# Performance work log

Measured on AMD Instinct MI355X. Metric: run time of the kernel, lower is better.

Reference implementation:

```python
import jax, jax.numpy as jnp
import numpy as np
import math

EMBED_DIM = 1024
NUM_HEADS = 16
HEAD_DIM = EMBED_DIM // NUM_HEADS


def setup_inputs() -> dict:
    key = jax.random.key(0)
    ks = jax.random.split(key, 5)
    s = 1.0 / math.sqrt(EMBED_DIM)
    return {
        "x": jax.random.normal(ks[0], (2, 2048, EMBED_DIM), dtype=jnp.float32),
        "w_qkv": jax.random.normal(ks[1], (EMBED_DIM, 3 * EMBED_DIM), dtype=jnp.float32) * s,
        "b_qkv": jax.random.normal(ks[2], (3 * EMBED_DIM,), dtype=jnp.float32) * 0.01,
        "w_proj": jax.random.normal(ks[3], (EMBED_DIM, EMBED_DIM), dtype=jnp.float32) * s,
        "b_proj": jax.random.normal(ks[4], (EMBED_DIM,), dtype=jnp.float32) * 0.01,
    }


def reference(x, w_qkv, b_qkv, w_proj, b_proj):
    B, T, C = x.shape
    qkv = (x @ w_qkv + b_qkv).reshape(B, T, 3, NUM_HEADS, HEAD_DIM)
    q, k, v = qkv[:, :, 0], qkv[:, :, 1], qkv[:, :, 2]  # [B,T,H,D]
    # scores: [B,H,T,T]
    att = jnp.einsum("bqhd,bkhd->bhqk", q, k) / math.sqrt(HEAD_DIM)
    causal = jnp.tril(jnp.ones((T, T), dtype=bool))
    att = jnp.where(causal[None, None], att, -jnp.inf)
    att = jax.nn.softmax(att, axis=-1)
    out = jnp.einsum("bhqk,bkhd->bqhd", att, v).reshape(B, T, C)
    return out @ w_proj + b_proj
```

## Files before the change

### kernel.cpp

```cpp
#include <hip/hip_runtime.h>
#include <stdint.h>


#define B_  2
#define T_  2048
#define C_  1024
#define NH  16
#define HD  64
#define BH_ (B_*NH)
#define M_  (B_*T_)

typedef __attribute__((ext_vector_type(8))) short short8;
typedef __attribute__((ext_vector_type(4))) float f32x4;
typedef __attribute__((ext_vector_type(4))) uint32_t u32x4;

struct frag2 { short8 hi, lo; };

typedef const __attribute__((address_space(1))) void* gas_ptr;
typedef __attribute__((address_space(3))) void* las_ptr;

__device__ __forceinline__ void gload_lds16(const void* g, void* l) {
  __builtin_amdgcn_global_load_lds((gas_ptr)g, (las_ptr)l, 16, 0, 0);
}

__device__ __forceinline__ uint32_t packsplit(float x) {
  uint32_t u = __float_as_uint(x);
  uint32_t hib = u & 0xffff0000u;
  float r = x - __uint_as_float(hib);
  uint32_t v = __float_as_uint(r);
  uint32_t lo = (v + 0x7fffu + ((v >> 16) & 1u)) >> 16;
  return hib | lo;
}

__device__ __forceinline__ frag2 extract2(u32x4 a, u32x4 b) {
  union U { u32x4 u; short8 s; };
  U H, L;
  H.u[0] = __builtin_amdgcn_perm(a[1], a[0], 0x07060302u);
  H.u[1] = __builtin_amdgcn_perm(a[3], a[2], 0x07060302u);
  H.u[2] = __builtin_amdgcn_perm(b[1], b[0], 0x07060302u);
  H.u[3] = __builtin_amdgcn_perm(b[3], b[2], 0x07060302u);
  L.u[0] = __builtin_amdgcn_perm(a[1], a[0], 0x05040100u);
  L.u[1] = __builtin_amdgcn_perm(a[3], a[2], 0x05040100u);
  L.u[2] = __builtin_amdgcn_perm(b[1], b[0], 0x05040100u);
  L.u[3] = __builtin_amdgcn_perm(b[3], b[2], 0x05040100u);
  frag2 f; f.hi = H.s; f.lo = L.s; return f;
}

__device__ __forceinline__ f32x4 mfma16(short8 a, short8 b, f32x4 c) {
  return __builtin_amdgcn_mfma_f32_16x16x32_bf16(a, b, c, 0, 0, 0);
}


__global__ __launch_bounds__(256) void pack4_kernel(const float4* __restrict__ in,
                                                    u32x4* __restrict__ out, int n4) {
  int i = blockIdx.x * 256 + threadIdx.x;
  if (i < n4) {
    float4 v = in[i];
    u32x4 p;
    p[0] = packsplit(v.x); p[1] = packsplit(v.y);
    p[2] = packsplit(v.z); p[3] = packsplit(v.w);
    out[i] = p;
  }
}

__global__ __launch_bounds__(1024) void pack_t_kernel(const float* __restrict__ in,
                                                      uint32_t* __restrict__ out, int R, int C) {
  __shared__ float tile[64][65];
  int c0 = blockIdx.x * 64, r0 = blockIdx.y * 64;
  int tx = threadIdx.x, ty = threadIdx.y;
  #pragma unroll
  for (int i = 0; i < 4; ++i)
    tile[ty + 16*i][tx] = in[(size_t)(r0 + ty + 16*i)*C + c0 + tx];
  __syncthreads();
  #pragma unroll
  for (int i = 0; i < 4; ++i)
    out[(size_t)(c0 + ty + 16*i)*R + r0 + tx] = packsplit(tile[tx][ty + 16*i]);
}


template<int MODE>
__global__ __launch_bounds__(256) void gemm_split(const uint32_t* __restrict__ A,
                                                  const uint32_t* __restrict__ Bt,
                                                  const float* __restrict__ bias,
                                                  uint32_t* __restrict__ qp,
                                                  uint32_t* __restrict__ kp,
                                                  uint32_t* __restrict__ vtp,
                                                  float* __restrict__ fout,
                                                  int M, int N, int K) {
  __shared__ uint32_t As[128*8*4];
  __shared__ uint32_t Bs[128*8*4];
  int tid = threadIdx.x;
  int w = tid >> 6, l = tid & 63, lg = l >> 4, lr = l & 15;
  int bm = blockIdx.y * 128, bn = blockIdx.x * 128;
  int wm = (w >> 1) * 64, wn = (w & 1) * 64;
  f32x4 zero = {0.f, 0.f, 0.f, 0.f};
  f32x4 acc[4][4];
  #pragma unroll
  for (int i = 0; i < 4; ++i)
    #pragma unroll
    for (int j = 0; j < 4; ++j) acc[i][j] = zero;

  for (int k0 = 0; k0 < K; k0 += 32) {
    #pragma unroll
    for (int i = 0; i < 4; ++i) {
      int s = tid + 256*i;
      int row = s >> 3, k4 = s & 7;
      int g4 = k4 ^ (row & 7);
      gload_lds16(A  + (size_t)(bm + row)*K + k0 + g4*4, &As[s*4]);
      gload_lds16(Bt + (size_t)(bn + row)*K + k0 + g4*4, &Bs[s*4]);
    }
    __syncthreads();
    frag2 af[4];
    #pragma unroll
    for (int mf = 0; mf < 4; ++mf) {
      int row = wm + mf*16 + lr;
      int sb = row*8;
      int s0 = sb + ((2*lg)   ^ (row & 7));
      int s1 = sb + ((2*lg+1) ^ (row & 7));
      af[mf] = extract2(*(const u32x4*)&As[s0*4], *(const u32x4*)&As[s1*4]);
    }
    #pragma unroll
    for (int nf = 0; nf < 4; ++nf) {
      int row = wn + nf*16 + lr;
      int sb = row*8;
      int s0 = sb + ((2*lg)   ^ (row & 7));
      int s1 = sb + ((2*lg+1) ^ (row & 7));
      frag2 bfr = extract2(*(const u32x4*)&Bs[s0*4], *(const u32x4*)&Bs[s1*4]);
      #pragma unroll
      for (int mf = 0; mf < 4; ++mf) {
        acc[mf][nf] = mfma16(af[mf].hi, bfr.hi, acc[mf][nf]);
        acc[mf][nf] = mfma16(af[mf].hi, bfr.lo, acc[mf][nf]);
        acc[mf][nf] = mfma16(af[mf].lo, bfr.hi, acc[mf][nf]);
      }
    }
    __syncthreads();
  }
  #pragma unroll
  for (int nf = 0; nf < 4; ++nf) {
    int col = bn + wn + nf*16 + lr;
    float bv = bias[col];
    #pragma unroll
    for (int mf = 0; mf < 4; ++mf) {
      #pragma unroll
      for (int r = 0; r < 4; ++r) {
        int rowm = bm + wm + mf*16 + lg*4 + r;
        float v = acc[mf][nf][r] + bv;
        if (MODE == 1) {
          fout[(size_t)rowm*N + col] = v;
        } else {
          int sec = col >> 10;
          int hh  = (col >> 6) & 15;
          int d   = col & 63;
          int b   = rowm >> 11, t = rowm & 2047;
          uint32_t pkv = packsplit(v);
          size_t bhh = (size_t)b*NH + hh;
          if (sec == 0)      qp[(bhh*T_ + t)*HD + d]  = pkv;
          else if (sec == 1) kp[(bhh*T_ + t)*HD + d]  = pkv;
          else               vtp[(bhh*HD + d)*T_ + t] = pkv;
        }
      }
    }
  }
}


__global__ __launch_bounds__(256) void attn_kernel(const uint32_t* __restrict__ qp,
                                                   const uint32_t* __restrict__ kp,
                                                   const uint32_t* __restrict__ vtp,
                                                   uint32_t* __restrict__ ctx) {
  __shared__ uint32_t Kt[64*16*4];
  __shared__ uint32_t Vt[64*16*4];
  __shared__ uint32_t Pl[4][16*68];
  int qt = blockIdx.x, bh = blockIdx.y;
  int tid = threadIdx.x;
  int w = tid >> 6, l = tid & 63, lg = l >> 4, lr = l & 15;
  int q0 = qt * 64;
  const uint32_t* qb = qp + ((size_t)bh*T_ + q0 + w*16 + lr)*HD;
  frag2 qf[2];
  #pragma unroll
  for (int ks = 0; ks < 2; ++ks) {
    u32x4 a = *(const u32x4*)(qb + ks*32 + lg*8);
    u32x4 b = *(const u32x4*)(qb + ks*32 + lg*8 + 4);
    qf[ks] = extract2(a, b);
  }
  f32x4 zero = {0.f, 0.f, 0.f, 0.f};
  f32x4 o[4] = {zero, zero, zero, zero};
  float m_r[4] = {-1e30f, -1e30f, -1e30f, -1e30f};
  float l_r[4] = {0.f, 0.f, 0.f, 0.f};
  uint32_t* pw = &Pl[w][0];

  for (int kt = 0; kt <= qt; ++kt) {
    int kv0 = kt * 64;
    #pragma unroll
    for (int i = 0; i < 4; ++i) {
      int s = tid + 256*i;
      int row = s >> 4, k4 = s & 15;
      int g4 = k4 ^ (row & 7);
      gload_lds16(kp  + ((size_t)bh*T_ + kv0 + row)*HD + g4*4, &Kt[s*4]);
      gload_lds16(vtp + ((size_t)bh*HD + row)*T_ + kv0 + g4*4, &Vt[s*4]);
    }
    __syncthreads();
    f32x4 s4[4];
    #pragma unroll
    for (int fc = 0; fc < 4; ++fc) {
      f32x4 acc = zero;
      #pragma unroll
      for (int ks = 0; ks < 2; ++ks) {
        int row = fc*16 + lr;
        int sb = row*16 + ks*8;
        int s0 = sb + ((2*lg)   ^ (row & 7));
        int s1 = sb + ((2*lg+1) ^ (row & 7));
        frag2 kf = extract2(*(const u32x4*)&Kt[s0*4], *(const u32x4*)&Kt[s1*4]);
        acc = mfma16(qf[ks].hi, kf.hi, acc);
        acc = mfma16(qf[ks].hi, kf.lo, acc);
        acc = mfma16(qf[ks].lo, kf.hi, acc);
      }
      s4[fc] = acc * 0.125f;
    }
    if (kt == qt) {
      #pragma unroll
      for (int fc = 0; fc < 4; ++fc)
        #pragma unroll
        for (int r = 0; r < 4; ++r) {
          int col = kv0 + fc*16 + lr;
          int rw  = q0 + w*16 + lg*4 + r;
          if (col > rw) s4[fc][r] = -1e30f;
        }
    }
    float sc[4];
    #pragma unroll
    for (int r = 0; r < 4; ++r) {
      float v = fmaxf(fmaxf(s4[0][r], s4[1][r]), fmaxf(s4[2][r], s4[3][r]));
      v = fmaxf(v, __shfl_xor(v, 1));
      v = fmaxf(v, __shfl_xor(v, 2));
      v = fmaxf(v, __shfl_xor(v, 4));
      v = fmaxf(v, __shfl_xor(v, 8));
      float mn = fmaxf(m_r[r], v);
      sc[r] = __expf(m_r[r] - mn);
      m_r[r] = mn;
    }
    float sum[4] = {0.f, 0.f, 0.f, 0.f};
    #pragma unroll
    for (int fc = 0; fc < 4; ++fc)
      #pragma unroll
      for (int r = 0; r < 4; ++r) {
        float p = __expf(s4[fc][r] - m_r[r]);
        s4[fc][r] = p;
        sum[r] += p;
      }
    #pragma unroll
    for (int r = 0; r < 4; ++r) {
      float v = sum[r];
      v += __shfl_xor(v, 1); v += __shfl_xor(v, 2);
      v += __shfl_xor(v, 4); v += __shfl_xor(v, 8);
      l_r[r] = l_r[r]*sc[r] + v;
    }
    #pragma unroll
    for (int df = 0; df < 4; ++df)
      #pragma unroll
      for (int r = 0; r < 4; ++r) o[df][r] *= sc[r];
    #pragma unroll
    for (int fc = 0; fc < 4; ++fc)
      #pragma unroll
      for (int r = 0; r < 4; ++r)
        pw[(lg*4 + r)*68 + fc*16 + lr] = packsplit(s4[fc][r]);
    __builtin_amdgcn_sched_barrier(0);
    frag2 pf[2];
    #pragma unroll
    for (int ks = 0; ks < 2; ++ks) {
      const uint32_t* pr = pw + lr*68 + ks*32 + lg*8;
      pf[ks] = extract2(*(const u32x4*)pr, *(const u32x4*)(pr + 4));
    }
    #pragma unroll
    for (int df = 0; df < 4; ++df) {
      #pragma unroll
      for (int ks = 0; ks < 2; ++ks) {
        int row = df*16 + lr;
        int sb = row*16 + ks*8;
        int s0 = sb + ((2*lg)   ^ (row & 7));
        int s1 = sb + ((2*lg+1) ^ (row & 7));
        frag2 vf = extract2(*(const u32x4*)&Vt[s0*4], *(const u32x4*)&Vt[s1*4]);
        o[df] = mfma16(pf[ks].hi, vf.hi, o[df]);
        o[df] = mfma16(pf[ks].hi, vf.lo, o[df]);
        o[df] = mfma16(pf[ks].lo, vf.hi, o[df]);
      }
    }
    __syncthreads();
  }
  int b = bh >> 4, h = bh & 15;
  float inv[4];
  #pragma unroll
  for (int r = 0; r < 4; ++r) inv[r] = 1.0f / l_r[r];
  #pragma unroll
  for (int df = 0; df < 4; ++df)
    #pragma unroll
    for (int r = 0; r < 4; ++r) {
      int q = q0 + w*16 + lg*4 + r;
      ctx[((size_t)b*T_ + q)*C_ + h*HD + df*16 + lr] = packsplit(o[df][r] * inv[r]);
    }
}


extern "C" void kernel_launch(void* const* d_in, const int* in_sizes, int n_in,
                              void* d_out, int out_size, void* d_ws, size_t ws_size,
                              hipStream_t stream) {
  (void)in_sizes; (void)n_in; (void)out_size; (void)ws_size;
  const float* x      = (const float*)d_in[0];
  const float* w_qkv  = (const float*)d_in[1];
  const float* b_qkv  = (const float*)d_in[2];
  const float* w_proj = (const float*)d_in[3];
  const float* b_proj = (const float*)d_in[4];
  float* out = (float*)d_out;

  uint8_t* ws = (uint8_t*)d_ws;
  const size_t MB = (size_t)1 << 20;
  uint32_t* xp  = (uint32_t*)(ws + 0);
  uint32_t* ctx = xp;
  uint32_t* wqt = (uint32_t*)(ws + 16*MB);
  uint32_t* wpt = (uint32_t*)(ws + 28*MB);
  uint32_t* qp  = (uint32_t*)(ws + 32*MB);
  uint32_t* kp  = (uint32_t*)(ws + 48*MB);
  uint32_t* vtp = (uint32_t*)(ws + 64*MB);

  pack4_kernel<<<(M_*C_/4 + 255)/256, 256, 0, stream>>>((const float4*)x, (u32x4*)xp, M_*C_/4);
  pack_t_kernel<<<dim3(3*C_/64, C_/64), dim3(64, 16), 0, stream>>>(w_qkv, wqt, C_, 3*C_);
  pack_t_kernel<<<dim3(C_/64, C_/64), dim3(64, 16), 0, stream>>>(w_proj, wpt, C_, C_);
  gemm_split<0><<<dim3(3*C_/128, M_/128), 256, 0, stream>>>(
      xp, wqt, b_qkv, qp, kp, vtp, nullptr, M_, 3*C_, C_);
  attn_kernel<<<dim3(T_/64, BH_), 256, 0, stream>>>(qp, kp, vtp, ctx);
  gemm_split<1><<<dim3(C_/128, M_/128), 256, 0, stream>>>(
      ctx, wpt, b_proj, nullptr, nullptr, nullptr, out, M_, C_, C_);
}
```

Before: 412.9 us.

## Store split-bf16 operands as separate hi/lo planes and double-buffer attention KV

Operands were packed as interleaved hi/lo bf16 pairs in 32-bit words and unpacked with perm instructions. They are now kept in separate hi and lo bf16 planes, so MFMA fragments load straight from LDS without extraction. The attention kernel also double-buffers K/V tiles in LDS, folds the 1/sqrt(d) scale into Q at the QKV epilogue, and remaps blocks so causal-heavy query tiles launch first with heads grouped per XCD. P is kept as fp32 in LDS and split using the hardware bf16 convert, at the cost of more LDS use and more separate 16-bit global stores.

```diff
diff --git a/kernel.cpp b/kernel.cpp
--- a/kernel.cpp
+++ b/kernel.cpp
@@ -14,8 +14,6 @@
 typedef __attribute__((ext_vector_type(4))) float f32x4;
 typedef __attribute__((ext_vector_type(4))) uint32_t u32x4;
 
-struct frag2 { short8 hi, lo; };
-
 typedef const __attribute__((address_space(1))) void* gas_ptr;
 typedef __attribute__((address_space(3))) void* las_ptr;
 
@@ -23,27 +21,40 @@
   __builtin_amdgcn_global_load_lds((gas_ptr)g, (las_ptr)l, 16, 0, 0);
 }
 
-__device__ __forceinline__ uint32_t packsplit(float x) {
-  uint32_t u = __float_as_uint(x);
-  uint32_t hib = u & 0xffff0000u;
-  float r = x - __uint_as_float(hib);
-  uint32_t v = __float_as_uint(r);
-  uint32_t lo = (v + 0x7fffu + ((v >> 16) & 1u)) >> 16;
-  return hib | lo;
-}
-
-__device__ __forceinline__ frag2 extract2(u32x4 a, u32x4 b) {
-  union U { u32x4 u; short8 s; };
-  U H, L;
+__device__ __forceinline__ unsigned short rne16(float x){
+  uint32_t v = __float_as_uint(x);
+  return (unsigned short)((v + 0x7fffu + ((v >> 16) & 1u)) >> 16);
+}
+
+__device__ __forceinline__ uint32_t cvtpk_bf16(float a, float b){
+  uint32_t r;
+  asm("v_cvt_pk_bf16_f32 %0, %1, %2" : "=v"(r) : "v"(a), "v"(b));
+  return r;
+}
+
+__device__ __forceinline__ short8 hi8(u32x4 a, u32x4 b){
+  union { u32x4 u; short8 s; } H;
   H.u[0] = __builtin_amdgcn_perm(a[1], a[0], 0x07060302u);
   H.u[1] = __builtin_amdgcn_perm(a[3], a[2], 0x07060302u);
   H.u[2] = __builtin_amdgcn_perm(b[1], b[0], 0x07060302u);
   H.u[3] = __builtin_amdgcn_perm(b[3], b[2], 0x07060302u);
-  L.u[0] = __builtin_amdgcn_perm(a[1], a[0], 0x05040100u);
-  L.u[1] = __builtin_amdgcn_perm(a[3], a[2], 0x05040100u);
-  L.u[2] = __builtin_amdgcn_perm(b[1], b[0], 0x05040100u);
-  L.u[3] = __builtin_amdgcn_perm(b[3], b[2], 0x05040100u);
-  frag2 f; f.hi = H.s; f.lo = L.s; return f;
+  return H.s;
+}
+__device__ __forceinline__ short8 lo8(u32x4 a, u32x4 b){
+  float l0 = __uint_as_float(a[0]) - __uint_as_float(a[0] & 0xffff0000u);
+  float l1 = __uint_as_float(a[1]) - __uint_as_float(a[1] & 0xffff0000u);
+  float l2 = __uint_as_float(a[2]) - __uint_as_float(a[2] & 0xffff0000u);
+  float l3 = __uint_as_float(a[3]) - __uint_as_float(a[3] & 0xffff0000u);
+  float l4 = __uint_as_float(b[0]) - __uint_as_float(b[0] & 0xffff0000u);
+  float l5 = __uint_as_float(b[1]) - __uint_as_float(b[1] & 0xffff0000u);
+  float l6 = __uint_as_float(b[2]) - __uint_as_float(b[2] & 0xffff0000u);
+  float l7 = __uint_as_float(b[3]) - __uint_as_float(b[3] & 0xffff0000u);
+  union { u32x4 u; short8 s; } L;
+  L.u[0] = cvtpk_bf16(l0, l1);
+  L.u[1] = cvtpk_bf16(l2, l3);
+  L.u[2] = cvtpk_bf16(l4, l5);
+  L.u[3] = cvtpk_bf16(l6, l7);
+  return L.s;
 }
 
 __device__ __forceinline__ f32x4 mfma16(short8 a, short8 b, f32x4 c) {
@@ -52,19 +63,31 @@
 
 
 __global__ __launch_bounds__(256) void pack4_kernel(const float4* __restrict__ in,
-                                                    u32x4* __restrict__ out, int n4) {
+                                                    unsigned short* __restrict__ oh,
+                                                    unsigned short* __restrict__ ol, int n4) {
   int i = blockIdx.x * 256 + threadIdx.x;
   if (i < n4) {
     float4 v = in[i];
-    u32x4 p;
-    p[0] = packsplit(v.x); p[1] = packsplit(v.y);
-    p[2] = packsplit(v.z); p[3] = packsplit(v.w);
-    out[i] = p;
+    float f[4] = {v.x, v.y, v.z, v.w};
+    ushort4 h, lo;
+    unsigned short hh[4], ll[4];
+    #pragma unroll
+    for (int j=0;j<4;++j){
+      uint32_t bt = __float_as_uint(f[j]);
+      hh[j] = (unsigned short)(bt >> 16);
+      ll[j] = rne16(f[j] - __uint_as_float(bt & 0xffff0000u));
+    }
+    h.x=hh[0]; h.y=hh[1]; h.z=hh[2]; h.w=hh[3];
+    lo.x=ll[0]; lo.y=ll[1]; lo.z=ll[2]; lo.w=ll[3];
+    *(ushort4*)(oh + (size_t)i*4) = h;
+    *(ushort4*)(ol + (size_t)i*4) = lo;
   }
 }
 
 __global__ __launch_bounds__(1024) void pack_t_kernel(const float* __restrict__ in,
-                                                      uint32_t* __restrict__ out, int R, int C) {
+                                                      unsigned short* __restrict__ oh,
+                                                      unsigned short* __restrict__ ol,
+                                                      int R, int C) {
   __shared__ float tile[64][65];
   int c0 = blockIdx.x * 64, r0 = blockIdx.y * 64;
   int tx = threadIdx.x, ty = threadIdx.y;
@@ -73,26 +96,46 @@
     tile[ty + 16*i][tx] = in[(size_t)(r0 + ty + 16*i)*C + c0 + tx];
   __syncthreads();
   #pragma unroll
-  for (int i = 0; i < 4; ++i)
-    out[(size_t)(c0 + ty + 16*i)*R + r0 + tx] = packsplit(tile[tx][ty + 16*i]);
+  for (int i = 0; i < 4; ++i) {
+    float v = tile[tx][ty + 16*i];
+    uint32_t bt = __float_as_uint(v);
+    size_t o = (size_t)(c0 + ty + 16*i)*R + r0 + tx;
+    oh[o] = (unsigned short)(bt >> 16);
+    ol[o] = rne16(v - __uint_as_float(bt & 0xffff0000u));
+  }
 }
 
 
 template<int MODE>
-__global__ __launch_bounds__(256) void gemm_split(const uint32_t* __restrict__ A,
-                                                  const uint32_t* __restrict__ Bt,
-                                                  const float* __restrict__ bias,
-                                                  uint32_t* __restrict__ qp,
-                                                  uint32_t* __restrict__ kp,
-                                                  uint32_t* __restrict__ vtp,
-                                                  float* __restrict__ fout,
-                                                  int M, int N, int K) {
-  __shared__ uint32_t As[128*8*4];
-  __shared__ uint32_t Bs[128*8*4];
+__global__ __launch_bounds__(256) void gemm_planes(
+    const unsigned short* __restrict__ Ah, const unsigned short* __restrict__ Al,
+    const unsigned short* __restrict__ Bh, const unsigned short* __restrict__ Bl,
+    const float* __restrict__ bias,
+    unsigned short* __restrict__ qh, unsigned short* __restrict__ ql,
+    unsigned short* __restrict__ kh, unsigned short* __restrict__ kl,
+    unsigned short* __restrict__ vth, unsigned short* __restrict__ vtl,
+    float* __restrict__ fout, int M, int N, int K) {
+  __shared__ unsigned short As[128*64];
+  __shared__ unsigned short Bs[128*64];
   int tid = threadIdx.x;
-  int w = tid >> 6, l = tid & 63, lg = l >> 4, lr = l & 15;
+  int w = tid >> 6, l = tid & 63, lg = l >> 4, lr = l & 15, lr7 = lr & 7;
   int bm = blockIdx.y * 128, bn = blockIdx.x * 128;
   int wm = (w >> 1) * 64, wn = (w & 1) * 64;
+
+  const unsigned short* asrc[4]; const unsigned short* bsrc[4];
+  #pragma unroll
+  for (int i = 0; i < 4; ++i) {
+    int s = tid + 256*i; int r = s >> 3, p = s & 7, u = p ^ (r & 7);
+    asrc[i] = ((u < 4) ? Ah : Al) + (size_t)(bm + r)*K + (u & 3)*8;
+    bsrc[i] = ((u < 4) ? Bh : Bl) + (size_t)(bn + r)*K + (u & 3)*8;
+  }
+  int aoh[4], boh[4];
+  #pragma unroll
+  for (int f = 0; f < 4; ++f) {
+    aoh[f] = (wm + f*16 + lr)*128 + ((lg ^ lr7)*16);
+    boh[f] = (wn + f*16 + lr)*128 + ((lg ^ lr7)*16);
+  }
+
   f32x4 zero = {0.f, 0.f, 0.f, 0.f};
   f32x4 acc[4][4];
   #pragma unroll
@@ -104,33 +147,26 @@
     #pragma unroll
     for (int i = 0; i < 4; ++i) {
       int s = tid + 256*i;
-      int row = s >> 3, k4 = s & 7;
-      int g4 = k4 ^ (row & 7);
-      gload_lds16(A  + (size_t)(bm + row)*K + k0 + g4*4, &As[s*4]);
-      gload_lds16(Bt + (size_t)(bn + row)*K + k0 + g4*4, &Bs[s*4]);
+      gload_lds16(asrc[i], (char*)As + (size_t)s*16);
+      gload_lds16(bsrc[i], (char*)Bs + (size_t)s*16);
+      asrc[i] += 32; bsrc[i] += 32;
     }
     __syncthreads();
-    frag2 af[4];
+    short8 ahf[4], alf[4];
     #pragma unroll
     for (int mf = 0; mf < 4; ++mf) {
-      int row = wm + mf*16 + lr;
-      int sb = row*8;
-      int s0 = sb + ((2*lg)   ^ (row & 7));
-      int s1 = sb + ((2*lg+1) ^ (row & 7));
-      af[mf] = extract2(*(const u32x4*)&As[s0*4], *(const u32x4*)&As[s1*4]);
+      ahf[mf] = *(const short8*)((const char*)As + aoh[mf]);
+      alf[mf] = *(const short8*)((const char*)As + (aoh[mf] ^ 64));
     }
     #pragma unroll
     for (int nf = 0; nf < 4; ++nf) {
-      int row = wn + nf*16 + lr;
-      int sb = row*8;
-      int s0 = sb + ((2*lg)   ^ (row & 7));
-      int s1 = sb + ((2*lg+1) ^ (row & 7));
-      frag2 bfr = extract2(*(const u32x4*)&Bs[s0*4], *(const u32x4*)&Bs[s1*4]);
+      short8 bhf = *(const short8*)((const char*)Bs + boh[nf]);
+      short8 blf = *(const short8*)((const char*)Bs + (boh[nf] ^ 64));
       #pragma unroll
       for (int mf = 0; mf < 4; ++mf) {
-        acc[mf][nf] = mfma16(af[mf].hi, bfr.hi, acc[mf][nf]);
-        acc[mf][nf] = mfma16(af[mf].hi, bfr.lo, acc[mf][nf]);
-        acc[mf][nf] = mfma16(af[mf].lo, bfr.hi, acc[mf][nf]);
+        acc[mf][nf] = mfma16(ahf[mf], bhf, acc[mf][nf]);
+        acc[mf][nf] = mfma16(ahf[mf], blf, acc[mf][nf]);
+        acc[mf][nf] = mfma16(alf[mf], bhf, acc[mf][nf]);
       }
     }
     __syncthreads();
@@ -152,11 +188,14 @@
           int hh  = (col >> 6) & 15;
           int d   = col & 63;
           int b   = rowm >> 11, t = rowm & 2047;
-          uint32_t pkv = packsplit(v);
           size_t bhh = (size_t)b*NH + hh;
-          if (sec == 0)      qp[(bhh*T_ + t)*HD + d]  = pkv;
-          else if (sec == 1) kp[(bhh*T_ + t)*HD + d]  = pkv;
-          else               vtp[(bhh*HD + d)*T_ + t] = pkv;
+          if (sec == 0) v *= 0.125f;
+          uint32_t bt = __float_as_uint(v);
+          unsigned short h16 = (unsigned short)(bt >> 16);
+          unsigned short l16 = rne16(v - __uint_as_float(bt & 0xffff0000u));
+          if (sec == 0)      { size_t o = (bhh*T_ + t)*HD + d;  qh[o] = h16;  ql[o] = l16; }
+          else if (sec == 1) { size_t o = (bhh*T_ + t)*HD + d;  kh[o] = h16;  kl[o] = l16; }
+          else               { size_t o = (bhh*HD + d)*T_ + t;  vth[o] = h16; vtl[o] = l16; }
         }
       }
     }
@@ -164,65 +203,106 @@
 }
 
 
-__global__ __launch_bounds__(256) void attn_kernel(const uint32_t* __restrict__ qp,
-                                                   const uint32_t* __restrict__ kp,
-                                                   const uint32_t* __restrict__ vtp,
-                                                   uint32_t* __restrict__ ctx) {
-  __shared__ uint32_t Kt[64*16*4];
-  __shared__ uint32_t Vt[64*16*4];
-  __shared__ uint32_t Pl[4][16*68];
-  int qt = blockIdx.x, bh = blockIdx.y;
+__global__ __launch_bounds__(256) void attn_kernel(
+    const unsigned short* __restrict__ qh, const unsigned short* __restrict__ ql,
+    const unsigned short* __restrict__ kh, const unsigned short* __restrict__ kl,
+    const unsigned short* __restrict__ vth, const unsigned short* __restrict__ vtl,
+    unsigned short* __restrict__ ctxh, unsigned short* __restrict__ ctxl) {
+  __shared__ unsigned short Kt[2][64*128];
+  __shared__ unsigned short Vt[2][64*128];
+  __shared__ float Pf[4][1024];
+  int bx = blockIdx.x;
+  int xcd = bx & 7, jj = bx >> 3;
+  int bh = xcd*4 + (jj >> 5);
+  int qt = 31 - (jj & 31);
   int tid = threadIdx.x;
-  int w = tid >> 6, l = tid & 63, lg = l >> 4, lr = l & 15;
+  int w = tid >> 6, l = tid & 63, lg = l >> 4, lr = l & 15, lr7 = lr & 7;
   int q0 = qt * 64;
-  const uint32_t* qb = qp + ((size_t)bh*T_ + q0 + w*16 + lr)*HD;
-  frag2 qf[2];
+
+  const unsigned short* qbh = qh + ((size_t)bh*T_ + q0 + w*16 + lr)*HD;
+  const unsigned short* qbl = ql + ((size_t)bh*T_ + q0 + w*16 + lr)*HD;
+  short8 qfh[2], qfl[2];
   #pragma unroll
   for (int ks = 0; ks < 2; ++ks) {
-    u32x4 a = *(const u32x4*)(qb + ks*32 + lg*8);
-    u32x4 b = *(const u32x4*)(qb + ks*32 + lg*8 + 4);
-    qf[ks] = extract2(a, b);
-  }
+    qfh[ks] = *(const short8*)(qbh + ks*32 + lg*8);
+    qfl[ks] = *(const short8*)(qbl + ks*32 + lg*8);
+  }
+
+  const unsigned short* ksrc[4]; const unsigned short* vsrc[4];
+  #pragma unroll
+  for (int i = 0; i < 4; ++i) {
+    int s = tid + 256*i; int r = s >> 4, p = s & 15;
+    int u = (p & 8) | ((p & 7) ^ (r & 7));
+    ksrc[i] = ((u < 8) ? kh : kl) + ((size_t)bh*T_ + r)*HD + (u & 7)*8;
+    vsrc[i] = ((u < 8) ? vth : vtl) + ((size_t)bh*HD + r)*T_ + (u & 7)*8;
+  }
+  auto stage = [&](int buf) {
+    #pragma unroll
+    for (int i = 0; i < 4; ++i) {
+      int s = tid + 256*i;
+      gload_lds16(ksrc[i], (char*)&Kt[buf][0] + (size_t)s*16);
+      gload_lds16(vsrc[i], (char*)&Vt[buf][0] + (size_t)s*16);
+    }
+    #pragma unroll
+    for (int i = 0; i < 4; ++i) { ksrc[i] += 64*HD; vsrc[i] += 64; }
+  };
+
+  int koff[4][2];
+  #pragma unroll
+  for (int fc = 0; fc < 4; ++fc)
+    #pragma unroll
+    for (int ks = 0; ks < 2; ++ks)
+      koff[fc][ks] = (fc*16 + lr)*256 + (((ks*4 + lg) ^ lr7)*16);
+  int pwoff[16];
+  #pragma unroll
+  for (int fc = 0; fc < 4; ++fc)
+    #pragma unroll
+    for (int r = 0; r < 4; ++r) {
+      int q = lg*4 + r;
+      int u = fc*4 + (lr >> 2);
+      pwoff[fc*4 + r] = q*256 + ((u ^ q)*16) + (lr & 3)*4;
+    }
+  int proff[2][2];
+  #pragma unroll
+  for (int ks = 0; ks < 2; ++ks)
+    #pragma unroll
+    for (int g = 0; g < 2; ++g)
+      proff[ks][g] = lr*256 + (((ks*8 + lg*2 + g) ^ lr)*16);
+
   f32x4 zero = {0.f, 0.f, 0.f, 0.f};
   f32x4 o[4] = {zero, zero, zero, zero};
   float m_r[4] = {-1e30f, -1e30f, -1e30f, -1e30f};
   float l_r[4] = {0.f, 0.f, 0.f, 0.f};
-  uint32_t* pw = &Pl[w][0];
+  char* PW = (char*)&Pf[w][0];
+
+  stage(0);
+  __syncthreads();
+  int cur = 0;
 
   for (int kt = 0; kt <= qt; ++kt) {
-    int kv0 = kt * 64;
-    #pragma unroll
-    for (int i = 0; i < 4; ++i) {
-      int s = tid + 256*i;
-      int row = s >> 4, k4 = s & 15;
-      int g4 = k4 ^ (row & 7);
-      gload_lds16(kp  + ((size_t)bh*T_ + kv0 + row)*HD + g4*4, &Kt[s*4]);
-      gload_lds16(vtp + ((size_t)bh*HD + row)*T_ + kv0 + g4*4, &Vt[s*4]);
-    }
-    __syncthreads();
+    if (kt < qt) stage(cur ^ 1);
+    const char* KB = (const char*)&Kt[cur][0];
+    const char* VB = (const char*)&Vt[cur][0];
     f32x4 s4[4];
     #pragma unroll
     for (int fc = 0; fc < 4; ++fc) {
       f32x4 acc = zero;
       #pragma unroll
       for (int ks = 0; ks < 2; ++ks) {
-        int row = fc*16 + lr;
-        int sb = row*16 + ks*8;
-        int s0 = sb + ((2*lg)   ^ (row & 7));
-        int s1 = sb + ((2*lg+1) ^ (row & 7));
-        frag2 kf = extract2(*(const u32x4*)&Kt[s0*4], *(const u32x4*)&Kt[s1*4]);
-        acc = mfma16(qf[ks].hi, kf.hi, acc);
-        acc = mfma16(qf[ks].hi, kf.lo, acc);
-        acc = mfma16(qf[ks].lo, kf.hi, acc);
+        short8 khf = *(const short8*)(KB + koff[fc][ks]);
+        short8 klf = *(const short8*)(KB + koff[fc][ks] + 128);
+        acc = mfma16(qfh[ks], khf, acc);
+        acc = mfma16(qfh[ks], klf, acc);
+        acc = mfma16(qfl[ks], khf, acc);
       }
-      s4[fc] = acc * 0.125f;
+      s4[fc] = acc;
     }
     if (kt == qt) {
       #pragma unroll
       for (int fc = 0; fc < 4; ++fc)
         #pragma unroll
         for (int r = 0; r < 4; ++r) {
-          int col = kv0 + fc*16 + lr;
+          int col = q0 + fc*16 + lr;
           int rw  = q0 + w*16 + lg*4 + r;
           if (col > rw) s4[fc][r] = -1e30f;
         }
@@ -263,29 +343,29 @@
     for (int fc = 0; fc < 4; ++fc)
       #pragma unroll
       for (int r = 0; r < 4; ++r)
-        pw[(lg*4 + r)*68 + fc*16 + lr] = packsplit(s4[fc][r]);
+        *(float*)(PW + pwoff[fc*4 + r]) = s4[fc][r];
     __builtin_amdgcn_sched_barrier(0);
-    frag2 pf[2];
+    short8 pah[2], pal[2];
     #pragma unroll
     for (int ks = 0; ks < 2; ++ks) {
-      const uint32_t* pr = pw + lr*68 + ks*32 + lg*8;
-      pf[ks] = extract2(*(const u32x4*)pr, *(const u32x4*)(pr + 4));
+      u32x4 a = *(const u32x4*)(PW + proff[ks][0]);
+      u32x4 b = *(const u32x4*)(PW + proff[ks][1]);
+      pah[ks] = hi8(a, b);
+      pal[ks] = lo8(a, b);
     }
     #pragma unroll
     for (int df = 0; df < 4; ++df) {
       #pragma unroll
       for (int ks = 0; ks < 2; ++ks) {
-        int row = df*16 + lr;
-        int sb = row*16 + ks*8;
-        int s0 = sb + ((2*lg)   ^ (row & 7));
-        int s1 = sb + ((2*lg+1) ^ (row & 7));
-        frag2 vf = extract2(*(const u32x4*)&Vt[s0*4], *(const u32x4*)&Vt[s1*4]);
-        o[df] = mfma16(pf[ks].hi, vf.hi, o[df]);
-        o[df] = mfma16(pf[ks].hi, vf.lo, o[df]);
-        o[df] = mfma16(pf[ks].lo, vf.hi, o[df]);
+        short8 vhf = *(const short8*)(VB + koff[df][ks]);
+        short8 vlf = *(const short8*)(VB + koff[df][ks] + 128);
+        o[df] = mfma16(pah[ks], vhf, o[df]);
+        o[df] = mfma16(pah[ks], vlf, o[df]);
+        o[df] = mfma16(pal[ks], vhf, o[df]);
       }
     }
     __syncthreads();
+    cur ^= 1;
   }
   int b = bh >> 4, h = bh & 15;
   float inv[4];
@@ -296,7 +376,11 @@
     #pragma unroll
     for (int r = 0; r < 4; ++r) {
       int q = q0 + w*16 + lg*4 + r;
-      ctx[((size_t)b*T_ + q)*C_ + h*HD + df*16 + lr] = packsplit(o[df][r] * inv[r]);
+      float v = o[df][r] * inv[r];
+      uint32_t bt = __float_as_uint(v);
+      size_t oo = ((size_t)b*T_ + q)*C_ + h*HD + df*16 + lr;
+      ctxh[oo] = (unsigned short)(bt >> 16);
+      ctxl[oo] = rne16(v - __uint_as_float(bt & 0xffff0000u));
     }
 }
 
@@ -314,20 +398,28 @@
 
   uint8_t* ws = (uint8_t*)d_ws;
   const size_t MB = (size_t)1 << 20;
-  uint32_t* xp  = (uint32_t*)(ws + 0);
-  uint32_t* ctx = xp;
-  uint32_t* wqt = (uint32_t*)(ws + 16*MB);
-  uint32_t* wpt = (uint32_t*)(ws + 28*MB);
-  uint32_t* qp  = (uint32_t*)(ws + 32*MB);
-  uint32_t* kp  = (uint32_t*)(ws + 48*MB);
-  uint32_t* vtp = (uint32_t*)(ws + 64*MB);
-
-  pack4_kernel<<<(M_*C_/4 + 255)/256, 256, 0, stream>>>((const float4*)x, (u32x4*)xp, M_*C_/4);
-  pack_t_kernel<<<dim3(3*C_/64, C_/64), dim3(64, 16), 0, stream>>>(w_qkv, wqt, C_, 3*C_);
-  pack_t_kernel<<<dim3(C_/64, C_/64), dim3(64, 16), 0, stream>>>(w_proj, wpt, C_, C_);
-  gemm_split<0><<<dim3(3*C_/128, M_/128), 256, 0, stream>>>(
-      xp, wqt, b_qkv, qp, kp, vtp, nullptr, M_, 3*C_, C_);
-  attn_kernel<<<dim3(T_/64, BH_), 256, 0, stream>>>(qp, kp, vtp, ctx);
-  gemm_split<1><<<dim3(C_/128, M_/128), 256, 0, stream>>>(
-      ctx, wpt, b_proj, nullptr, nullptr, nullptr, out, M_, C_, C_);
-}
+  unsigned short* xh  = (unsigned short*)(ws + 0);
+  unsigned short* xl  = (unsigned short*)(ws + 8*MB);
+  unsigned short* cth = xh;
+  unsigned short* ctl = xl;
+  unsigned short* wqh = (unsigned short*)(ws + 16*MB);
+  unsigned short* wql = (unsigned short*)(ws + 22*MB);
+  unsigned short* wph = (unsigned short*)(ws + 28*MB);
+  unsigned short* wpl = (unsigned short*)(ws + 30*MB);
+  unsigned short* qhp = (unsigned short*)(ws + 32*MB);
+  unsigned short* qlp = (unsigned short*)(ws + 40*MB);
+  unsigned short* khp = (unsigned short*)(ws + 48*MB);
+  unsigned short* klp = (unsigned short*)(ws + 56*MB);
+  unsigned short* vth = (unsigned short*)(ws + 64*MB);
+  unsigned short* vtl = (unsigned short*)(ws + 72*MB);
+
+  pack4_kernel<<<(M_*C_/4 + 255)/256, 256, 0, stream>>>((const float4*)x, xh, xl, M_*C_/4);
+  pack_t_kernel<<<dim3(3*C_/64, C_/64), dim3(64, 16), 0, stream>>>(w_qkv, wqh, wql, C_, 3*C_);
+  pack_t_kernel<<<dim3(C_/64, C_/64), dim3(64, 16), 0, stream>>>(w_proj, wph, wpl, C_, C_);
+  gemm_planes<0><<<dim3(3*C_/128, M_/128), 256, 0, stream>>>(
+      xh, xl, wqh, wql, b_qkv, qhp, qlp, khp, klp, vth, vtl, nullptr, M_, 3*C_, C_);
+  attn_kernel<<<dim3(1024), 256, 0, stream>>>(qhp, qlp, khp, klp, vth, vtl, cth, ctl);
+  gemm_planes<1><<<dim3(C_/128, M_/128), 256, 0, stream>>>(
+      cth, ctl, wph, wpl, b_proj, nullptr, nullptr, nullptr, nullptr, nullptr, nullptr,
+      out, M_, C_, C_);
+}
```

After: 384.1 us. -7.0%, faster.
